# Kernel tuning notes

Measured on AMD Instinct MI355X. Metric: run time of the kernel, lower is better.

The kernel has to match this reference:

```python
import jax, jax.numpy as jnp
import numpy as np

DIM = 1024
HEADS = 16
DIM_HEAD = 64
INNER = HEADS * DIM_HEAD
SCALE = DIM_HEAD ** -0.5
CAUSAL = True


def setup_inputs() -> dict:
    key = jax.random.key(0)
    k1, k2, k3, k4 = jax.random.split(key, 4)
    b, n = 4, 2048
    x = jax.random.normal(k1, (b, n, DIM), dtype=jnp.float32)
    mask = jnp.ones((b, n), dtype=bool)
    w_qkv = jax.random.normal(k2, (DIM, 3 * INNER), dtype=jnp.float32) * (DIM ** -0.5)
    w_out = jax.random.normal(k3, (INNER, DIM), dtype=jnp.float32) * (INNER ** -0.5)
    ln_g = jnp.ones((DIM,), dtype=jnp.float32)
    return {"x": x, "mask": mask, "w_qkv": w_qkv, "w_out": w_out, "ln_g": ln_g}


def clip_layernorm(x, g):
    eps = 1e-5 if x.dtype == jnp.float32 else 1e-3
    mean = jnp.mean(x, axis=-1, keepdims=True)
    var = jnp.var(x, axis=-1, keepdims=True)  # unbiased=False
    return (x - mean) * jax.lax.rsqrt(var + eps) * g


def reference(x, mask, w_qkv, w_out, ln_g):
    b, n, _ = x.shape
    qkv = x @ w_qkv  # [b, n, 3*inner]
    q, k, v = jnp.split(qkv, 3, axis=-1)
    split_heads = lambda t: t.reshape(b, n, HEADS, DIM_HEAD).transpose(0, 2, 1, 3)
    q, k, v = split_heads(q), split_heads(k), split_heads(v)
    q = q * SCALE
    sim = jnp.einsum('bhid,bhjd->bhij', q, k)
    mask_value = -jnp.finfo(sim.dtype).max
    sim = jnp.where(mask[:, None, None, :], sim, mask_value)
    if CAUSAL:
        causal_mask = jnp.triu(jnp.ones((n, n), dtype=bool), k=1)
        sim = jnp.where(causal_mask, mask_value, sim)
    attn = jax.nn.softmax(sim.astype(jnp.float32), axis=-1).astype(sim.dtype)
    out = jnp.einsum('bhij,bhjd->bhid', attn, v)
    out = out.transpose(0, 2, 1, 3).reshape(b, n, INNER)
    out = out @ w_out
    return clip_layernorm(out, ln_g)
```

## Files before the change

### kernel.cpp

```cpp
#include <hip/hip_runtime.h>


typedef unsigned short u16;
typedef __attribute__((ext_vector_type(8))) short bf16x8;
typedef __attribute__((ext_vector_type(4))) float f32x4;
typedef __attribute__((ext_vector_type(4))) unsigned short u16x4;
typedef __attribute__((ext_vector_type(2))) unsigned u32x2;

#define B_SZ  4
#define NSEQ  2048
#define DIMM  1024
#define NQKV  3072
#define MROWS 8192

#define AS_GLOBAL __attribute__((address_space(1)))
#define AS_LDS    __attribute__((address_space(3)))

__device__ __forceinline__ void async_copy16(void* lds, const void* g) {
  __builtin_amdgcn_global_load_lds((const AS_GLOBAL void*)g, (AS_LDS void*)lds, 16, 0, 0);
}

__device__ __forceinline__ u16 f32_to_bf16(float f) {
  unsigned u = __float_as_uint(f);
  u += 0x7FFFu + ((u >> 16) & 1u);
  return (u16)(u >> 16);
}

__device__ __forceinline__ unsigned cvt_pk_bf16(float a, float b) {
  unsigned r;
  asm("v_cvt_pk_bf16_f32 %0, %1, %2" : "=v"(r) : "v"(a), "v"(b));
  return r;
}


__global__ __launch_bounds__(256) void cvt_bf16_k(const float* __restrict__ in,
                                                  u16* __restrict__ out, int n4) {
  int i = blockIdx.x * 256 + threadIdx.x;
  if (i >= n4) return;
  f32x4 v = ((const f32x4*)in)[i];
  u16x4 o;
  #pragma unroll
  for (int c = 0; c < 4; ++c) o[c] = f32_to_bf16(v[c]);
  ((u16x4*)out)[i] = o;
}

__global__ __launch_bounds__(256) void tconv_k(const float* __restrict__ in,
                                               u16* __restrict__ out, int K, int N) {
  __shared__ float tile[64][65];
  int n0 = blockIdx.x * 64, k0 = blockIdx.y * 64;
  int t = threadIdx.x, tr = t >> 6, tc = t & 63;
  #pragma unroll
  for (int i = 0; i < 16; ++i)
    tile[tr + i * 4][tc] = in[(size_t)(k0 + tr + i * 4) * N + n0 + tc];
  __syncthreads();
  #pragma unroll
  for (int i = 0; i < 16; ++i)
    out[(size_t)(n0 + tr + i * 4) * K + k0 + tc] = f32_to_bf16(tile[tc][tr + i * 4]);
}


__device__ __forceinline__ void gemm_tile(const u16* __restrict__ A, const u16* __restrict__ Bt,
                                          int K, size_t arow0, size_t brow0,
                                          u16* lA, u16* lB, int t, f32x4 acc[4][4]) {
  const int w = t >> 6, l = t & 63;
  const int wr = (w >> 1) * 64, wc = (w & 1) * 64;
  const int l4 = l >> 4, l15 = l & 15;

  const int r0 = t >> 2;
  const int r1 = 64 + (t >> 2);
  const int c3 = t & 3;
  const int sc0 = c3 ^ ((r0 >> 1) & 3);
  const int sc1 = c3 ^ ((r1 >> 1) & 3);

  auto stage = [&](int kt, int bufi) {
    u16* dA = lA + bufi * 4096;
    u16* dB = lB + bufi * 4096;
    async_copy16(&dA[(size_t)t * 8],         &A[(arow0 + r0) * (size_t)K + kt + sc0 * 8]);
    async_copy16(&dA[(size_t)(256 + t) * 8], &A[(arow0 + r1) * (size_t)K + kt + sc1 * 8]);
    async_copy16(&dB[(size_t)t * 8],         &Bt[(brow0 + r0) * (size_t)K + kt + sc0 * 8]);
    async_copy16(&dB[(size_t)(256 + t) * 8], &Bt[(brow0 + r1) * (size_t)K + kt + sc1 * 8]);
  };

  const int cs = l4 ^ ((l15 >> 1) & 3);

  auto step = [&](int bufi) {
    const u16* bA = lA + bufi * 4096;
    const u16* bB = lB + bufi * 4096;
    bf16x8 af[4], bfr[4];
    #pragma unroll
    for (int i = 0; i < 4; ++i) af[i] = *(const bf16x8*)&bA[(wr + i * 16 + l15) * 32 + cs * 8];
    #pragma unroll
    for (int j = 0; j < 4; ++j) bfr[j] = *(const bf16x8*)&bB[(wc + j * 16 + l15) * 32 + cs * 8];
    __builtin_amdgcn_s_setprio(1);
    #pragma unroll
    for (int i = 0; i < 4; ++i)
      #pragma unroll
      for (int j = 0; j < 4; ++j)
        acc[i][j] = __builtin_amdgcn_mfma_f32_16x16x32_bf16(af[i], bfr[j], acc[i][j], 0, 0, 0);
    __builtin_amdgcn_s_setprio(0);
  };

  const int T = K >> 5;
  stage(0, 0);
  stage(32, 1);
  int bc = 0, bn = 2;
  for (int s = 0; s < T - 2; ++s) {
    asm volatile("s_waitcnt vmcnt(4)" ::: "memory");
    __builtin_amdgcn_s_barrier();
    __builtin_amdgcn_sched_barrier(0);
    stage((s + 2) * 32, bn);
    step(bc);
    bc = bc == 2 ? 0 : bc + 1;
    bn = bn == 2 ? 0 : bn + 1;
  }
  asm volatile("s_waitcnt vmcnt(4)" ::: "memory");
  __builtin_amdgcn_s_barrier();
  __builtin_amdgcn_sched_barrier(0);
  step(bc);
  bc = bc == 2 ? 0 : bc + 1;
  asm volatile("s_waitcnt vmcnt(0)" ::: "memory");
  __builtin_amdgcn_s_barrier();
  __builtin_amdgcn_sched_barrier(0);
  step(bc);
}

__global__ __launch_bounds__(256) void gemm_qkv_k(const u16* __restrict__ A, const u16* __restrict__ Bt,
                                                  u16* __restrict__ qb, u16* __restrict__ kb,
                                                  u16* __restrict__ vtb) {
  __shared__ u16 lA[12288], lB[12288];
  f32x4 acc[4][4];
  #pragma unroll
  for (int i = 0; i < 4; ++i)
    #pragma unroll
    for (int j = 0; j < 4; ++j) acc[i][j] = (f32x4){0.f, 0.f, 0.f, 0.f};
  const int t = threadIdx.x;
  gemm_tile(A, Bt, DIMM, (size_t)blockIdx.y * 128, (size_t)blockIdx.x * 128, lA, lB, t, acc);
  const int w = t >> 6, l = t & 63;
  const int wr = (w >> 1) * 64, wc = (w & 1) * 64;
  const int l4 = l >> 4, l15 = l & 15;
  const float QSCALE = 0.125f * 1.44269504089f;
  #pragma unroll
  for (int i = 0; i < 4; ++i)
    #pragma unroll
    for (int j = 0; j < 4; ++j)
      #pragma unroll
      for (int r = 0; r < 4; ++r) {
        int row = blockIdx.y * 128 + wr + i * 16 + l4 * 4 + r;
        int col = blockIdx.x * 128 + wc + j * 16 + l15;
        float v = acc[i][j][r];
        int bb = row >> 11, nr = row & 2047;
        int part = col >> 10, rem = col & 1023;
        int h = rem >> 6, d = rem & 63;
        int bh = bb * 16 + h;
        if (part == 0)      qb[((size_t)bh * NSEQ + nr) * 64 + d] = f32_to_bf16(v * QSCALE);
        else if (part == 1) kb[((size_t)bh * NSEQ + nr) * 64 + d] = f32_to_bf16(v);
        else                vtb[((size_t)bh * 64 + d) * NSEQ + nr] = f32_to_bf16(v);
      }
}

__global__ __launch_bounds__(256) void gemm_out_k(const u16* __restrict__ A, const u16* __restrict__ Bt,
                                                  float* __restrict__ C) {
  __shared__ u16 lA[12288], lB[12288];
  f32x4 acc[4][4];
  #pragma unroll
  for (int i = 0; i < 4; ++i)
    #pragma unroll
    for (int j = 0; j < 4; ++j) acc[i][j] = (f32x4){0.f, 0.f, 0.f, 0.f};
  const int t = threadIdx.x;
  gemm_tile(A, Bt, DIMM, (size_t)blockIdx.y * 128, (size_t)blockIdx.x * 128, lA, lB, t, acc);
  const int w = t >> 6, l = t & 63;
  const int wr = (w >> 1) * 64, wc = (w & 1) * 64;
  const int l4 = l >> 4, l15 = l & 15;
  #pragma unroll
  for (int i = 0; i < 4; ++i)
    #pragma unroll
    for (int j = 0; j < 4; ++j)
      #pragma unroll
      for (int r = 0; r < 4; ++r) {
        int row = blockIdx.y * 128 + wr + i * 16 + l4 * 4 + r;
        int col = blockIdx.x * 128 + wc + j * 16 + l15;
        C[(size_t)row * DIMM + col] = acc[i][j][r];
      }
}


__global__ __launch_bounds__(512, 4) void attn_k(const u16* __restrict__ qb, const u16* __restrict__ kb,
                                                 const u16* __restrict__ vtb, u16* __restrict__ ao) {
  __shared__ u16 lK[2][64 * 64];
  __shared__ u16 lV[2][64 * 64];
  __shared__ u16 lP[8][16 * 64];
  const int bh = blockIdx.y;
  const int t = threadIdx.x, w = t >> 6, l = t & 63;
  const int l4 = l >> 4, l15 = l & 15;
  const int b = bh >> 4, h = bh & 15;
  u16* lPw = lP[w];

  const int srow = t >> 3;
  const int ssc = (t & 7) ^ (srow & 7);

  #pragma unroll 1
  for (int phase = 0; phase < 2; ++phase) {
    const int qt = phase == 0 ? (int)blockIdx.x : 15 - (int)blockIdx.x;
    const int q0w = qt * 128 + w * 16;

    bf16x8 qf0 = *(const bf16x8*)&qb[((size_t)bh * NSEQ + q0w + l15) * 64 + l4 * 8];
    bf16x8 qf1 = *(const bf16x8*)&qb[((size_t)bh * NSEQ + q0w + l15) * 64 + 32 + l4 * 8];

    float m_r = -1e30f, l_r = 0.f;
    f32x4 o[4];
    #pragma unroll
    for (int d = 0; d < 4; ++d) o[d] = (f32x4){0.f, 0.f, 0.f, 0.f};

    const int njt = 2 * qt + 2;

    {
      async_copy16(&lK[0][t * 8], &kb[((size_t)bh * NSEQ + srow) * 64 + ssc * 8]);
      async_copy16(&lV[0][t * 8], &vtb[((size_t)bh * 64 + srow) * NSEQ + ssc * 8]);
    }
    int buf = 0;

    for (int jt = 0; jt < njt; ++jt) {
      __syncthreads();
      if (jt + 1 < njt) {
        int bsel = buf ^ 1, jn = jt + 1;
        async_copy16(&lK[bsel][t * 8], &kb[((size_t)bh * NSEQ + jn * 64 + srow) * 64 + ssc * 8]);
        async_copy16(&lV[bsel][t * 8], &vtb[((size_t)bh * 64 + srow) * NSEQ + (size_t)jn * 64 + ssc * 8]);
      }
      const int jt64 = jt * 64;
      if (jt64 > q0w + 15) { buf ^= 1; continue; }
      const u16* Kb = lK[buf];
      const u16* Vb = lV[buf];

      bf16x8 kf[4][2];
      #pragma unroll
      for (int nf = 0; nf < 4; ++nf)
        #pragma unroll
        for (int kk = 0; kk < 2; ++kk)
          kf[nf][kk] = *(const bf16x8*)&Kb[(nf * 16 + l15) * 64 + ((kk * 4 + l4) ^ (l15 & 7)) * 8];

      f32x4 z[4];
      __builtin_amdgcn_s_setprio(1);
      #pragma unroll
      for (int nf = 0; nf < 4; ++nf) {
        f32x4 zz = (f32x4){0.f, 0.f, 0.f, 0.f};
        zz = __builtin_amdgcn_mfma_f32_16x16x32_bf16(kf[nf][0], qf0, zz, 0, 0, 0);
        zz = __builtin_amdgcn_mfma_f32_16x16x32_bf16(kf[nf][1], qf1, zz, 0, 0, 0);
        z[nf] = zz;
      }
      __builtin_amdgcn_s_setprio(0);

      bf16x8 bv[4][2];
      #pragma unroll
      for (int dd = 0; dd < 4; ++dd)
        #pragma unroll
        for (int kk = 0; kk < 2; ++kk)
          bv[dd][kk] = *(const bf16x8*)&Vb[(dd * 16 + l15) * 64 + ((kk * 4 + l4) ^ (l15 & 7)) * 8];

      if (jt64 + 63 > q0w) {
        #pragma unroll
        for (int nf = 0; nf < 4; ++nf)
          #pragma unroll
          for (int r = 0; r < 4; ++r)
            if (jt64 + nf * 16 + l4 * 4 + r > q0w + l15) z[nf][r] = -1e30f;
      }

      float mt = fmaxf(fmaxf(z[0][0], z[0][1]), fmaxf(z[0][2], z[0][3]));
      #pragma unroll
      for (int nf = 1; nf < 4; ++nf)
        mt = fmaxf(mt, fmaxf(fmaxf(z[nf][0], z[nf][1]), fmaxf(z[nf][2], z[nf][3])));
      mt = fmaxf(mt, __shfl_xor(mt, 16));
      mt = fmaxf(mt, __shfl_xor(mt, 32));

      if (!__all(mt <= m_r + 8.f)) {
        float nm = fmaxf(m_r, mt);
        float sc = __builtin_amdgcn_exp2f(m_r - nm);
        m_r = nm;
        l_r *= sc;
        float scr[4];
        #pragma unroll
        for (int r = 0; r < 4; ++r) scr[r] = __shfl(sc, l4 * 4 + r);
        #pragma unroll
        for (int d = 0; d < 4; ++d)
          #pragma unroll
          for (int r = 0; r < 4; ++r) o[d][r] *= scr[r];
      }

      float rs = 0.f;
      unsigned pk[4][2];
      #pragma unroll
      for (int nf = 0; nf < 4; ++nf)
        #pragma unroll
        for (int hh = 0; hh < 2; ++hh) {
          float p0 = __builtin_amdgcn_exp2f(z[nf][2 * hh]     - m_r);
          float p1 = __builtin_amdgcn_exp2f(z[nf][2 * hh + 1] - m_r);
          rs += p0 + p1;
          pk[nf][hh] = cvt_pk_bf16(p0, p1);
        }
      rs += __shfl_xor(rs, 16);
      rs += __shfl_xor(rs, 32);
      l_r += rs;

      #pragma unroll
      for (int nf = 0; nf < 4; ++nf) {
        int u = (2 * nf + (l4 >> 1)) ^ (l15 & 7);
        *(u32x2*)&lPw[l15 * 64 + u * 8 + (l4 & 1) * 4] = (u32x2){pk[nf][0], pk[nf][1]};
      }
      __builtin_amdgcn_sched_barrier(0);
      int u0 = l4 ^ (l15 & 7), u1 = (4 + l4) ^ (l15 & 7);
      bf16x8 af0 = *(const bf16x8*)&lPw[l15 * 64 + u0 * 8];
      bf16x8 af1 = *(const bf16x8*)&lPw[l15 * 64 + u1 * 8];

      __builtin_amdgcn_s_setprio(1);
      #pragma unroll
      for (int d = 0; d < 4; ++d) {
        o[d] = __builtin_amdgcn_mfma_f32_16x16x32_bf16(af0, bv[d][0], o[d], 0, 0, 0);
        o[d] = __builtin_amdgcn_mfma_f32_16x16x32_bf16(af1, bv[d][1], o[d], 0, 0, 0);
      }
      __builtin_amdgcn_s_setprio(0);
      buf ^= 1;
    }

    float lv[4];
    #pragma unroll
    for (int r = 0; r < 4; ++r) lv[r] = __shfl(l_r, l4 * 4 + r);
    #pragma unroll
    for (int d = 0; d < 4; ++d)
      #pragma unroll
      for (int r = 0; r < 4; ++r) {
        int nrow = q0w + l4 * 4 + r;
        float vv = o[d][r] / lv[r];
        ao[((size_t)(b * NSEQ + nrow)) * 1024 + h * 64 + d * 16 + l15] = f32_to_bf16(vv);
      }
  }
}

__global__ __launch_bounds__(256) void ln_k(float* __restrict__ io, const float* __restrict__ g) {
  const int row = blockIdx.x, t = threadIdx.x;
  const int w = t >> 6, l = t & 63;
  f32x4 v = ((const f32x4*)(io + (size_t)row * DIMM))[t];
  float s = v[0] + v[1] + v[2] + v[3];
  float q = v[0] * v[0] + v[1] * v[1] + v[2] * v[2] + v[3] * v[3];
  #pragma unroll
  for (int off = 1; off < 64; off <<= 1) { s += __shfl_xor(s, off); q += __shfl_xor(q, off); }
  __shared__ float ss[8];
  if (l == 0) { ss[w] = s; ss[4 + w] = q; }
  __syncthreads();
  s = ss[0] + ss[1] + ss[2] + ss[3];
  q = ss[4] + ss[5] + ss[6] + ss[7];
  float mean = s * (1.f / DIMM);
  float var = q * (1.f / DIMM) - mean * mean;
  float rstd = rsqrtf(var + 1e-5f);
  f32x4 gv = ((const f32x4*)g)[t];
  f32x4 y;
  #pragma unroll
  for (int c = 0; c < 4; ++c) y[c] = (v[c] - mean) * rstd * gv[c];
  ((f32x4*)(io + (size_t)row * DIMM))[t] = y;
}

extern "C" void kernel_launch(void* const* d_in, const int* in_sizes, int n_in,
                              void* d_out, int out_size, void* d_ws, size_t ws_size,
                              hipStream_t stream) {
  const float* x     = (const float*)d_in[0];
  const float* w_qkv = (const float*)d_in[2];
  const float* w_out = (const float*)d_in[3];
  const float* ln_g  = (const float*)d_in[4];
  float* out = (float*)d_out;

  char* ws = (char*)d_ws;
  const size_t MB = 1u << 20;
  u16* x_bf   = (u16*)(ws);
  u16* wqkv_t = (u16*)(ws + 16 * MB);
  u16* wout_t = (u16*)(ws + 22 * MB);
  u16* qb     = (u16*)(ws + 24 * MB);
  u16* kb     = (u16*)(ws + 40 * MB);
  u16* vtb    = (u16*)(ws + 56 * MB);
  u16* attn_o = x_bf;

  cvt_bf16_k<<<8192, 256, 0, stream>>>(x, x_bf, (MROWS * DIMM) / 4);
  tconv_k<<<dim3(NQKV / 64, DIMM / 64), 256, 0, stream>>>(w_qkv, wqkv_t, DIMM, NQKV);
  tconv_k<<<dim3(DIMM / 64, DIMM / 64), 256, 0, stream>>>(w_out, wout_t, DIMM, DIMM);
  gemm_qkv_k<<<dim3(NQKV / 128, MROWS / 128), 256, 0, stream>>>(x_bf, wqkv_t, qb, kb, vtb);
  attn_k<<<dim3(8, B_SZ * 16), 512, 0, stream>>>(qb, kb, vtb, attn_o);
  gemm_out_k<<<dim3(DIMM / 128, MROWS / 128), 256, 0, stream>>>(attn_o, wout_t, out);
  ln_k<<<MROWS, 256, 0, stream>>>(out, ln_g);
}
```

Measured before the change: 207.6 us.

## Process paired causal query tiles in one K/V sweep and fuse prep kernels

The attention kernel now loads K/V tiles once per key block and feeds them to both paired query tiles (early and late), where before it ran two sequential phases that each streamed K/V separately. This halves LDS staging and the global K/V traffic for the short tile. The three conversion and transpose kernels are merged into one launch to save launch overhead. Block order is also interleaved, and launch bounds are relaxed to two blocks per CU because the extra accumulators raise register pressure, which may lower occupancy.

```diff
diff --git a/kernel.cpp b/kernel.cpp
--- a/kernel.cpp
+++ b/kernel.cpp
@@ -33,22 +33,9 @@
 }
 
 
-__global__ __launch_bounds__(256) void cvt_bf16_k(const float* __restrict__ in,
-                                                  u16* __restrict__ out, int n4) {
-  int i = blockIdx.x * 256 + threadIdx.x;
-  if (i >= n4) return;
-  f32x4 v = ((const f32x4*)in)[i];
-  u16x4 o;
-  #pragma unroll
-  for (int c = 0; c < 4; ++c) o[c] = f32_to_bf16(v[c]);
-  ((u16x4*)out)[i] = o;
-}
-
-__global__ __launch_bounds__(256) void tconv_k(const float* __restrict__ in,
-                                               u16* __restrict__ out, int K, int N) {
-  __shared__ float tile[64][65];
-  int n0 = blockIdx.x * 64, k0 = blockIdx.y * 64;
-  int t = threadIdx.x, tr = t >> 6, tc = t & 63;
+__device__ __forceinline__ void tconv_body(const float* __restrict__ in, u16* __restrict__ out,
+                                           int K, int N, int n0, int k0, float (*tile)[65], int t) {
+  int tr = t >> 6, tc = t & 63;
   #pragma unroll
   for (int i = 0; i < 16; ++i)
     tile[tr + i * 4][tc] = in[(size_t)(k0 + tr + i * 4) * N + n0 + tc];
@@ -56,6 +43,27 @@
   #pragma unroll
   for (int i = 0; i < 16; ++i)
     out[(size_t)(n0 + tr + i * 4) * K + k0 + tc] = f32_to_bf16(tile[tc][tr + i * 4]);
+}
+
+__global__ __launch_bounds__(256) void pre_k(const float* __restrict__ x, u16* __restrict__ x_bf,
+                                             const float* __restrict__ wqkv, u16* __restrict__ wqkv_t,
+                                             const float* __restrict__ wout, u16* __restrict__ wout_t) {
+  __shared__ float tile[64][65];
+  const int bidx = blockIdx.x, t = threadIdx.x;
+  if (bidx < 8192) {
+    int i = bidx * 256 + t;
+    f32x4 v = ((const f32x4*)x)[i];
+    u16x4 o;
+    #pragma unroll
+    for (int c = 0; c < 4; ++c) o[c] = f32_to_bf16(v[c]);
+    ((u16x4*)x_bf)[i] = o;
+  } else if (bidx < 8960) {
+    int id = bidx - 8192;
+    tconv_body(wqkv, wqkv_t, DIMM, NQKV, (id % 48) * 64, (id / 48) * 64, tile, t);
+  } else {
+    int id = bidx - 8960;
+    tconv_body(wout, wout_t, DIMM, DIMM, (id % 16) * 64, (id / 16) * 64, tile, t);
+  }
 }
 
 
@@ -184,11 +192,13 @@
 }
 
 
-__global__ __launch_bounds__(512, 4) void attn_k(const u16* __restrict__ qb, const u16* __restrict__ kb,
+__global__ __launch_bounds__(512, 2) void attn_k(const u16* __restrict__ qb, const u16* __restrict__ kb,
                                                  const u16* __restrict__ vtb, u16* __restrict__ ao) {
   __shared__ u16 lK[2][64 * 64];
   __shared__ u16 lV[2][64 * 64];
   __shared__ u16 lP[8][16 * 64];
+  const int xx = (int)blockIdx.x;
+  const int p = (xx & 1) ? 7 - (xx >> 1) : (xx >> 1);
   const int bh = blockIdx.y;
   const int t = threadIdx.x, w = t >> 6, l = t & 63;
   const int l4 = l >> 4, l15 = l & 15;
@@ -198,128 +208,134 @@
   const int srow = t >> 3;
   const int ssc = (t & 7) ^ (srow & 7);
 
+  const int q0A = p * 128 + w * 16;
+  const int q0B = (15 - p) * 128 + w * 16;
+
+  bf16x8 qfA0 = *(const bf16x8*)&qb[((size_t)bh * NSEQ + q0A + l15) * 64 + l4 * 8];
+  bf16x8 qfA1 = *(const bf16x8*)&qb[((size_t)bh * NSEQ + q0A + l15) * 64 + 32 + l4 * 8];
+  bf16x8 qfB0 = *(const bf16x8*)&qb[((size_t)bh * NSEQ + q0B + l15) * 64 + l4 * 8];
+  bf16x8 qfB1 = *(const bf16x8*)&qb[((size_t)bh * NSEQ + q0B + l15) * 64 + 32 + l4 * 8];
+
+  float mA = -1e30f, lAs = 0.f, mB = -1e30f, lBs = 0.f;
+  f32x4 oA[4], oB[4];
+  #pragma unroll
+  for (int d = 0; d < 4; ++d) { oA[d] = (f32x4){0.f, 0.f, 0.f, 0.f}; oB[d] = (f32x4){0.f, 0.f, 0.f, 0.f}; }
+
+  const int njtB = 2 * (15 - p) + 2;
+
+  async_copy16(&lK[0][t * 8], &kb[((size_t)bh * NSEQ + srow) * 64 + ssc * 8]);
+  async_copy16(&lV[0][t * 8], &vtb[((size_t)bh * 64 + srow) * NSEQ + ssc * 8]);
+  int buf = 0;
+
+  bf16x8 kf[4][2], bv[4][2];
+
+  auto body = [&](bf16x8 qf0, bf16x8 qf1, int q0w, int jt64,
+                  float& m_r, float& l_r, f32x4 (&o)[4]) {
+    f32x4 z[4];
+    __builtin_amdgcn_s_setprio(1);
+    #pragma unroll
+    for (int nf = 0; nf < 4; ++nf) {
+      f32x4 zz = (f32x4){0.f, 0.f, 0.f, 0.f};
+      zz = __builtin_amdgcn_mfma_f32_16x16x32_bf16(kf[nf][0], qf0, zz, 0, 0, 0);
+      zz = __builtin_amdgcn_mfma_f32_16x16x32_bf16(kf[nf][1], qf1, zz, 0, 0, 0);
+      z[nf] = zz;
+    }
+    __builtin_amdgcn_s_setprio(0);
+
+    if (jt64 + 63 > q0w) {
+      #pragma unroll
+      for (int nf = 0; nf < 4; ++nf)
+        #pragma unroll
+        for (int r = 0; r < 4; ++r)
+          if (jt64 + nf * 16 + l4 * 4 + r > q0w + l15) z[nf][r] = -1e30f;
+    }
+
+    float mt = fmaxf(fmaxf(z[0][0], z[0][1]), fmaxf(z[0][2], z[0][3]));
+    #pragma unroll
+    for (int nf = 1; nf < 4; ++nf)
+      mt = fmaxf(mt, fmaxf(fmaxf(z[nf][0], z[nf][1]), fmaxf(z[nf][2], z[nf][3])));
+    mt = fmaxf(mt, __shfl_xor(mt, 16));
+    mt = fmaxf(mt, __shfl_xor(mt, 32));
+
+    if (!__all(mt <= m_r + 8.f)) {
+      float nm = fmaxf(m_r, mt);
+      float sc = __builtin_amdgcn_exp2f(m_r - nm);
+      m_r = nm;
+      l_r *= sc;
+      float scr[4];
+      #pragma unroll
+      for (int r = 0; r < 4; ++r) scr[r] = __shfl(sc, l4 * 4 + r);
+      #pragma unroll
+      for (int d = 0; d < 4; ++d)
+        #pragma unroll
+        for (int r = 0; r < 4; ++r) o[d][r] *= scr[r];
+    }
+
+    float rs = 0.f;
+    unsigned pk[4][2];
+    #pragma unroll
+    for (int nf = 0; nf < 4; ++nf)
+      #pragma unroll
+      for (int hh = 0; hh < 2; ++hh) {
+        float p0 = __builtin_amdgcn_exp2f(z[nf][2 * hh]     - m_r);
+        float p1 = __builtin_amdgcn_exp2f(z[nf][2 * hh + 1] - m_r);
+        rs += p0 + p1;
+        pk[nf][hh] = cvt_pk_bf16(p0, p1);
+      }
+    rs += __shfl_xor(rs, 16);
+    rs += __shfl_xor(rs, 32);
+    l_r += rs;
+
+    #pragma unroll
+    for (int nf = 0; nf < 4; ++nf) {
+      int u = (2 * nf + (l4 >> 1)) ^ (l15 & 7);
+      *(u32x2*)&lPw[l15 * 64 + u * 8 + (l4 & 1) * 4] = (u32x2){pk[nf][0], pk[nf][1]};
+    }
+    __builtin_amdgcn_sched_barrier(0);
+    int u0 = l4 ^ (l15 & 7), u1 = (4 + l4) ^ (l15 & 7);
+    bf16x8 af0 = *(const bf16x8*)&lPw[l15 * 64 + u0 * 8];
+    bf16x8 af1 = *(const bf16x8*)&lPw[l15 * 64 + u1 * 8];
+
+    __builtin_amdgcn_s_setprio(1);
+    #pragma unroll
+    for (int d = 0; d < 4; ++d) {
+      o[d] = __builtin_amdgcn_mfma_f32_16x16x32_bf16(af0, bv[d][0], o[d], 0, 0, 0);
+      o[d] = __builtin_amdgcn_mfma_f32_16x16x32_bf16(af1, bv[d][1], o[d], 0, 0, 0);
+    }
+    __builtin_amdgcn_s_setprio(0);
+  };
+
   #pragma unroll 1
-  for (int phase = 0; phase < 2; ++phase) {
-    const int qt = phase == 0 ? (int)blockIdx.x : 15 - (int)blockIdx.x;
-    const int q0w = qt * 128 + w * 16;
-
-    bf16x8 qf0 = *(const bf16x8*)&qb[((size_t)bh * NSEQ + q0w + l15) * 64 + l4 * 8];
-    bf16x8 qf1 = *(const bf16x8*)&qb[((size_t)bh * NSEQ + q0w + l15) * 64 + 32 + l4 * 8];
-
-    float m_r = -1e30f, l_r = 0.f;
-    f32x4 o[4];
-    #pragma unroll
-    for (int d = 0; d < 4; ++d) o[d] = (f32x4){0.f, 0.f, 0.f, 0.f};
-
-    const int njt = 2 * qt + 2;
-
-    {
-      async_copy16(&lK[0][t * 8], &kb[((size_t)bh * NSEQ + srow) * 64 + ssc * 8]);
-      async_copy16(&lV[0][t * 8], &vtb[((size_t)bh * 64 + srow) * NSEQ + ssc * 8]);
-    }
-    int buf = 0;
-
-    for (int jt = 0; jt < njt; ++jt) {
-      __syncthreads();
-      if (jt + 1 < njt) {
-        int bsel = buf ^ 1, jn = jt + 1;
-        async_copy16(&lK[bsel][t * 8], &kb[((size_t)bh * NSEQ + jn * 64 + srow) * 64 + ssc * 8]);
-        async_copy16(&lV[bsel][t * 8], &vtb[((size_t)bh * 64 + srow) * NSEQ + (size_t)jn * 64 + ssc * 8]);
-      }
-      const int jt64 = jt * 64;
-      if (jt64 > q0w + 15) { buf ^= 1; continue; }
+  for (int jt = 0; jt < njtB; ++jt) {
+    __syncthreads();
+    if (jt + 1 < njtB) {
+      int bsel = buf ^ 1, jn = jt + 1;
+      async_copy16(&lK[bsel][t * 8], &kb[((size_t)bh * NSEQ + jn * 64 + srow) * 64 + ssc * 8]);
+      async_copy16(&lV[bsel][t * 8], &vtb[((size_t)bh * 64 + srow) * NSEQ + (size_t)jn * 64 + ssc * 8]);
+    }
+    const int jt64 = jt * 64;
+    const bool actA = (jt64 <= q0A + 15);
+    const bool actB = (jt64 <= q0B + 15);
+    if (actA || actB) {
       const u16* Kb = lK[buf];
       const u16* Vb = lV[buf];
-
-      bf16x8 kf[4][2];
       #pragma unroll
       for (int nf = 0; nf < 4; ++nf)
         #pragma unroll
         for (int kk = 0; kk < 2; ++kk)
           kf[nf][kk] = *(const bf16x8*)&Kb[(nf * 16 + l15) * 64 + ((kk * 4 + l4) ^ (l15 & 7)) * 8];
-
-      f32x4 z[4];
-      __builtin_amdgcn_s_setprio(1);
-      #pragma unroll
-      for (int nf = 0; nf < 4; ++nf) {
-        f32x4 zz = (f32x4){0.f, 0.f, 0.f, 0.f};
-        zz = __builtin_amdgcn_mfma_f32_16x16x32_bf16(kf[nf][0], qf0, zz, 0, 0, 0);
-        zz = __builtin_amdgcn_mfma_f32_16x16x32_bf16(kf[nf][1], qf1, zz, 0, 0, 0);
-        z[nf] = zz;
-      }
-      __builtin_amdgcn_s_setprio(0);
-
-      bf16x8 bv[4][2];
       #pragma unroll
       for (int dd = 0; dd < 4; ++dd)
         #pragma unroll
         for (int kk = 0; kk < 2; ++kk)
           bv[dd][kk] = *(const bf16x8*)&Vb[(dd * 16 + l15) * 64 + ((kk * 4 + l4) ^ (l15 & 7)) * 8];
-
-      if (jt64 + 63 > q0w) {
-        #pragma unroll
-        for (int nf = 0; nf < 4; ++nf)
-          #pragma unroll
-          for (int r = 0; r < 4; ++r)
-            if (jt64 + nf * 16 + l4 * 4 + r > q0w + l15) z[nf][r] = -1e30f;
-      }
-
-      float mt = fmaxf(fmaxf(z[0][0], z[0][1]), fmaxf(z[0][2], z[0][3]));
-      #pragma unroll
-      for (int nf = 1; nf < 4; ++nf)
-        mt = fmaxf(mt, fmaxf(fmaxf(z[nf][0], z[nf][1]), fmaxf(z[nf][2], z[nf][3])));
-      mt = fmaxf(mt, __shfl_xor(mt, 16));
-      mt = fmaxf(mt, __shfl_xor(mt, 32));
-
-      if (!__all(mt <= m_r + 8.f)) {
-        float nm = fmaxf(m_r, mt);
-        float sc = __builtin_amdgcn_exp2f(m_r - nm);
-        m_r = nm;
-        l_r *= sc;
-        float scr[4];
-        #pragma unroll
-        for (int r = 0; r < 4; ++r) scr[r] = __shfl(sc, l4 * 4 + r);
-        #pragma unroll
-        for (int d = 0; d < 4; ++d)
-          #pragma unroll
-          for (int r = 0; r < 4; ++r) o[d][r] *= scr[r];
-      }
-
-      float rs = 0.f;
-      unsigned pk[4][2];
-      #pragma unroll
-      for (int nf = 0; nf < 4; ++nf)
-        #pragma unroll
-        for (int hh = 0; hh < 2; ++hh) {
-          float p0 = __builtin_amdgcn_exp2f(z[nf][2 * hh]     - m_r);
-          float p1 = __builtin_amdgcn_exp2f(z[nf][2 * hh + 1] - m_r);
-          rs += p0 + p1;
-          pk[nf][hh] = cvt_pk_bf16(p0, p1);
-        }
-      rs += __shfl_xor(rs, 16);
-      rs += __shfl_xor(rs, 32);
-      l_r += rs;
-
-      #pragma unroll
-      for (int nf = 0; nf < 4; ++nf) {
-        int u = (2 * nf + (l4 >> 1)) ^ (l15 & 7);
-        *(u32x2*)&lPw[l15 * 64 + u * 8 + (l4 & 1) * 4] = (u32x2){pk[nf][0], pk[nf][1]};
-      }
-      __builtin_amdgcn_sched_barrier(0);
-      int u0 = l4 ^ (l15 & 7), u1 = (4 + l4) ^ (l15 & 7);
-      bf16x8 af0 = *(const bf16x8*)&lPw[l15 * 64 + u0 * 8];
-      bf16x8 af1 = *(const bf16x8*)&lPw[l15 * 64 + u1 * 8];
-
-      __builtin_amdgcn_s_setprio(1);
-      #pragma unroll
-      for (int d = 0; d < 4; ++d) {
-        o[d] = __builtin_amdgcn_mfma_f32_16x16x32_bf16(af0, bv[d][0], o[d], 0, 0, 0);
-        o[d] = __builtin_amdgcn_mfma_f32_16x16x32_bf16(af1, bv[d][1], o[d], 0, 0, 0);
-      }
-      __builtin_amdgcn_s_setprio(0);
-      buf ^= 1;
-    }
-
+      if (actB) body(qfB0, qfB1, q0B, jt64, mB, lBs, oB);
+      if (actA) body(qfA0, qfA1, q0A, jt64, mA, lAs, oA);
+    }
+    buf ^= 1;
+  }
+
+  auto epi = [&](float l_r, f32x4 (&o)[4], int q0w) {
     float lv[4];
     #pragma unroll
     for (int r = 0; r < 4; ++r) lv[r] = __shfl(l_r, l4 * 4 + r);
@@ -331,7 +347,9 @@
         float vv = o[d][r] / lv[r];
         ao[((size_t)(b * NSEQ + nrow)) * 1024 + h * 64 + d * 16 + l15] = f32_to_bf16(vv);
       }
-  }
+  };
+  epi(lBs, oB, q0B);
+  epi(lAs, oA, q0A);
 }
 
 __global__ __launch_bounds__(256) void ln_k(float* __restrict__ io, const float* __restrict__ g) {
@@ -376,9 +394,7 @@
   u16* vtb    = (u16*)(ws + 56 * MB);
   u16* attn_o = x_bf;
 
-  cvt_bf16_k<<<8192, 256, 0, stream>>>(x, x_bf, (MROWS * DIMM) / 4);
-  tconv_k<<<dim3(NQKV / 64, DIMM / 64), 256, 0, stream>>>(w_qkv, wqkv_t, DIMM, NQKV);
-  tconv_k<<<dim3(DIMM / 64, DIMM / 64), 256, 0, stream>>>(w_out, wout_t, DIMM, DIMM);
+  pre_k<<<9216, 256, 0, stream>>>(x, x_bf, w_qkv, wqkv_t, w_out, wout_t);
   gemm_qkv_k<<<dim3(NQKV / 128, MROWS / 128), 256, 0, stream>>>(x_bf, wqkv_t, qb, kb, vtb);
   attn_k<<<dim3(8, B_SZ * 16), 512, 0, stream>>>(qb, kb, vtb, attn_o);
   gemm_out_k<<<dim3(DIMM / 128, MROWS / 128), 256, 0, stream>>>(attn_o, wout_t, out);
```

New measurement: 232.6 us. +12.0%, slower.
